# Optimization experiments

Measured on AMD Instinct MI355X. Metric: run time of the kernel, lower is better.

## Reference

```python
import jax, jax.numpy as jnp
import numpy as np

H, LQ, LK, DK, DV = 16, 2048, 2048, 64, 64


def setup_inputs() -> dict:
    key = jax.random.key(0)
    k1, k2, k3, k4 = jax.random.split(key, 4)
    q = jax.random.normal(k1, (H, LQ, DK), dtype=jnp.float32)
    k = jax.random.normal(k2, (H, LK, DK), dtype=jnp.float32)
    v = jax.random.normal(k3, (1, LK, DV), dtype=jnp.float32)
    attn_mask = jax.random.randint(k4, (H, LQ, LK), 0, 2) == 1
    return {"q": q, "k": k, "v": v, "attn_mask": attn_mask, "train_attn": 1}


def reference(q, k, v, attn_mask, train_attn):
    scale = jnp.asarray(np.sqrt(q.shape[-1]), q.dtype)  # sqrt(d_k)
    # [H, Lq, Lk] scores
    attn = jnp.einsum('hqd,hkd->hqk', q, k) / scale
    attn = jnp.where(attn_mask, -jnp.inf, attn)
    attn = jax.nn.softmax(attn, axis=-1)
    # torch: v.repeat(n_heads,1,1) then bmm -> v[0] broadcast over heads
    attn_used = attn if train_attn else jax.lax.stop_gradient(attn)
    v_used = jax.lax.stop_gradient(v) if train_attn else v
    outputs = jnp.einsum('hqk,kd->hqd', attn_used, v_used[0])
    return outputs, attn
```

## Files before the change

### kernel.cpp

```cpp
#include <hip/hip_runtime.h>
#include <hip/hip_bf16.h>
#include <math.h>

#define H_ 16
#define LQ_ 2048
#define LK_ 2048
#define D_ 64
#define QB_ 16
#define NW_ 4
#define STRIP_ (LK_ / NW_)
#define NTL_ (STRIP_ / 16)
#define NCH_ (STRIP_ / 32)
#define PP_ 40

using bf16x8  = __attribute__((ext_vector_type(8))) short;
using floatx4 = __attribute__((ext_vector_type(4))) float;

__device__ __forceinline__ unsigned short f2bf(float x) {
  unsigned u = __builtin_bit_cast(unsigned, x);
  return (unsigned short)((u + 0x7fffu + ((u >> 16) & 1u)) >> 16);
}
__device__ __forceinline__ float bf2f(unsigned short b) {
  return __builtin_bit_cast(float, ((unsigned)b) << 16);
}
__device__ __forceinline__ void hilo8(const float* __restrict__ x, bf16x8& hv, bf16x8& lv) {
#pragma unroll
  for (int j = 0; j < 8; ++j) {
    unsigned short hb = f2bf(x[j]);
    float d = x[j] - bf2f(hb);
    hv[j] = (short)hb;
    lv[j] = (short)(unsigned short)(__builtin_bit_cast(unsigned, d) >> 16);
  }
}

__global__ void detect_mask_kernel(const unsigned* __restrict__ m, int* __restrict__ flag) {
  const int l = (int)threadIdx.x;
  unsigned acc = 0;
#pragma unroll
  for (int i = 0; i < 4; ++i) acc |= m[l * 4 + i];
  unsigned long long any = __ballot(acc & 0xFFFFFF00u);
  if (l == 0) *flag = any ? 1 : 0;
}

__global__ void pack_mask_kernel(const void* __restrict__ Mg, const int* __restrict__ flagp,
                                 unsigned* __restrict__ Wp) {
  const size_t i = (size_t)blockIdx.x * 256 + threadIdx.x;
  unsigned wbits = 0;
  if (*flagp) {
    const uint4* p = (const uint4*)((const unsigned char*)Mg + i * 32);
    uint4 a = p[0], b = p[1];
    unsigned v[8] = {a.x, a.y, a.z, a.w, b.x, b.y, b.z, b.w};
#pragma unroll
    for (int k = 0; k < 8; ++k)
#pragma unroll
      for (int bb = 0; bb < 4; ++bb)
        wbits |= (((v[k] >> (8 * bb)) & 0xFFu) ? 1u : 0u) << (4 * k + bb);
  } else {
    const uint4* p = (const uint4*)((const int*)Mg + i * 32);
#pragma unroll
    for (int k = 0; k < 8; ++k) {
      uint4 a = p[k];
      wbits |= (a.x ? 1u : 0u) << (4 * k)     | (a.y ? 1u : 0u) << (4 * k + 1) |
               (a.z ? 1u : 0u) << (4 * k + 2) | (a.w ? 1u : 0u) << (4 * k + 3);
    }
  }
  Wp[i] = wbits;
}

__global__ void conv_hilo_kernel(const float* __restrict__ X,
                                 unsigned short* __restrict__ Hh,
                                 unsigned short* __restrict__ Hl) {
  const size_t i = (size_t)blockIdx.x * 256 + threadIdx.x;
  float x[8];
  *(floatx4*)x       = *(const floatx4*)(X + i * 8);
  *(floatx4*)(x + 4) = *(const floatx4*)(X + i * 8 + 4);
  bf16x8 hv, lv;
  hilo8(x, hv, lv);
  *(bf16x8*)(Hh + i * 8) = hv;
  *(bf16x8*)(Hl + i * 8) = lv;
}

__global__ void conv_vt_kernel(const float* __restrict__ V,
                               unsigned short* __restrict__ Th,
                               unsigned short* __restrict__ Tl) {
  const int i = (int)(blockIdx.x * 256 + threadIdx.x);
  const int d = i >> 11, k = i & 2047;
  float x = V[(size_t)k * D_ + d];
  unsigned short hb = f2bf(x);
  float rem = x - bf2f(hb);
  Th[(size_t)d * LK_ + k] = hb;
  Tl[(size_t)d * LK_ + k] = (unsigned short)(__builtin_bit_cast(unsigned, rem) >> 16);
}

template <bool PRE>
__global__ __launch_bounds__(256, 2)
void attn_sp_kernel(const float* __restrict__ Qg, const float* __restrict__ Kg,
                    const float* __restrict__ Vg, const void* __restrict__ Mg,
                    const int* __restrict__ flagp,
                    const unsigned* __restrict__ Wp,
                    const unsigned short* __restrict__ Qhp, const unsigned short* __restrict__ Qlp,
                    const unsigned short* __restrict__ Khp, const unsigned short* __restrict__ Klp,
                    const unsigned short* __restrict__ Vthp, const unsigned short* __restrict__ Vtlp,
                    float* __restrict__ Og, float* __restrict__ Ag) {
  const int tid = (int)threadIdx.x;
  const int l = tid & 63, w = tid >> 6, lm = l & 15, lg = l >> 4;
  const int hd = (int)blockIdx.y;
  const int q0 = (int)blockIdx.x * QB_;
  const int k0 = w * STRIP_;

  __shared__ float SM_[NW_][QB_];
  __shared__ float SS_[NW_][QB_];
  __shared__ __align__(16) float OM[NW_][QB_ * D_];
  __shared__ __align__(16) unsigned short Pb[NW_][2][QB_ * PP_];

  const int maskByte = PRE ? 0 : *flagp;
  const unsigned char* Mb = (const unsigned char*)Mg;
  const int* Mi = (const int*)Mg;

  bf16x8 qh[2], ql[2];
  if constexpr (PRE) {
    const unsigned short* qp  = Qhp + ((size_t)hd * LQ_ + q0 + lm) * D_;
    const unsigned short* qp2 = Qlp + ((size_t)hd * LQ_ + q0 + lm) * D_;
    qh[0] = *(const bf16x8*)(qp + lg * 8);       qh[1] = *(const bf16x8*)(qp + 32 + lg * 8);
    ql[0] = *(const bf16x8*)(qp2 + lg * 8);      ql[1] = *(const bf16x8*)(qp2 + 32 + lg * 8);
  } else {
    const float* qp = Qg + ((size_t)hd * LQ_ + q0 + lm) * D_;
#pragma unroll
    for (int s = 0; s < 2; ++s) {
      float x[8];
      *(floatx4*)x       = *(const floatx4*)(qp + s * 32 + lg * 8);
      *(floatx4*)(x + 4) = *(const floatx4*)(qp + s * 32 + lg * 8 + 4);
      hilo8(x, qh[s], ql[s]);
    }
  }

  float s[NTL_][4];
  unsigned wm[4];
  const size_t mwrow = ((size_t)hd * LQ_ + q0 + lg * 4);
#pragma unroll
  for (int t = 0; t < NTL_; ++t) {
    if constexpr (PRE) {
      if ((t & 1) == 0) {
#pragma unroll
        for (int j = 0; j < 4; ++j)
          wm[j] = Wp[((mwrow + j) << 6) + (size_t)(w * 16) + (t >> 1)];
      }
    }
    bf16x8 kh[2], kl[2];
    if constexpr (PRE) {
      const unsigned short* kp  = Khp + ((size_t)hd * LK_ + k0 + t * 16 + lm) * D_;
      const unsigned short* kp2 = Klp + ((size_t)hd * LK_ + k0 + t * 16 + lm) * D_;
      kh[0] = *(const bf16x8*)(kp + lg * 8);       kh[1] = *(const bf16x8*)(kp + 32 + lg * 8);
      kl[0] = *(const bf16x8*)(kp2 + lg * 8);      kl[1] = *(const bf16x8*)(kp2 + 32 + lg * 8);
    } else {
      const float* kp = Kg + ((size_t)hd * LK_ + k0 + t * 16 + lm) * D_;
#pragma unroll
      for (int ss = 0; ss < 2; ++ss) {
        float x[8];
        *(floatx4*)x       = *(const floatx4*)(kp + ss * 32 + lg * 8);
        *(floatx4*)(x + 4) = *(const floatx4*)(kp + ss * 32 + lg * 8 + 4);
        hilo8(x, kh[ss], kl[ss]);
      }
    }
    floatx4 acc = {0.f, 0.f, 0.f, 0.f};
#pragma unroll
    for (int ss = 0; ss < 2; ++ss) {
      acc = __builtin_amdgcn_mfma_f32_16x16x32_bf16(qh[ss], kh[ss], acc, 0, 0, 0);
      acc = __builtin_amdgcn_mfma_f32_16x16x32_bf16(ql[ss], kh[ss], acc, 0, 0, 0);
      acc = __builtin_amdgcn_mfma_f32_16x16x32_bf16(qh[ss], kl[ss], acc, 0, 0, 0);
    }
#pragma unroll
    for (int j = 0; j < 4; ++j) {
      int mk;
      if constexpr (PRE) {
        mk = (int)((wm[j] >> ((t & 1) * 16 + lm)) & 1u);
      } else {
        const size_t mi = ((size_t)hd * LQ_ + q0 + lg * 4 + j) * (size_t)LK_ + k0 + t * 16 + lm;
        mk = maskByte ? (int)Mb[mi] : Mi[mi];
      }
      s[t][j] = mk ? -1e30f : acc[j] * 0.125f;
    }
  }

  float mf[4];
#pragma unroll
  for (int j = 0; j < 4; ++j) {
    float m = s[0][j];
#pragma unroll
    for (int t = 1; t < NTL_; ++t) m = fmaxf(m, s[t][j]);
#pragma unroll
    for (int off = 1; off <= 8; off <<= 1) m = fmaxf(m, __shfl_xor(m, off, 64));
    if (lm == 0) SM_[w][lg * 4 + j] = m;
  }
  __syncthreads();
#pragma unroll
  for (int j = 0; j < 4; ++j)
    mf[j] = fmaxf(fmaxf(SM_[0][lg * 4 + j], SM_[1][lg * 4 + j]),
                  fmaxf(SM_[2][lg * 4 + j], SM_[3][lg * 4 + j]));
#pragma unroll
  for (int j = 0; j < 4; ++j) {
    float sum = 0.f;
#pragma unroll
    for (int t = 0; t < NTL_; ++t) {
      float p = __expf(s[t][j] - mf[j]);
      s[t][j] = p;
      sum += p;
    }
#pragma unroll
    for (int off = 1; off <= 8; off <<= 1) sum += __shfl_xor(sum, off, 64);
    if (lm == 0) SS_[w][lg * 4 + j] = sum;
  }
  __syncthreads();
  float inv[4];
#pragma unroll
  for (int j = 0; j < 4; ++j)
    inv[j] = 1.0f / (SS_[0][lg * 4 + j] + SS_[1][lg * 4 + j] +
                     SS_[2][lg * 4 + j] + SS_[3][lg * 4 + j]);

  floatx4 oacc[4];
#pragma unroll
  for (int n = 0; n < 4; ++n) oacc[n] = {0.f, 0.f, 0.f, 0.f};
  unsigned short* PhL = &Pb[w][0][0];
  unsigned short* PlL = &Pb[w][1][0];

#pragma unroll
  for (int c = 0; c < NCH_; ++c) {
#pragma unroll
    for (int u = 0; u < 2; ++u) {
#pragma unroll
      for (int j = 0; j < 4; ++j) {
        const float p = s[2 * c + u][j] * inv[j];
        const unsigned short hb = f2bf(p);
        const float rem = p - bf2f(hb);
        PhL[(lg * 4 + j) * PP_ + u * 16 + lm] = hb;
        PlL[(lg * 4 + j) * PP_ + u * 16 + lm] =
            (unsigned short)(__builtin_bit_cast(unsigned, rem) >> 16);
      }
    }
    const bf16x8 pa  = *(const bf16x8*)(PhL + lm * PP_ + lg * 8);
    const bf16x8 plo = *(const bf16x8*)(PlL + lm * PP_ + lg * 8);

    {
      float pr[8];
#pragma unroll
      for (int jj = 0; jj < 8; ++jj)
        pr[jj] = bf2f((unsigned short)pa[jj]) + bf2f((unsigned short)plo[jj]);
      float* arow = Ag + ((size_t)hd * LQ_ + q0 + lm) * (size_t)LK_ + k0 + c * 32 + lg * 8;
      floatx4 v0 = {pr[0], pr[1], pr[2], pr[3]};
      floatx4 v1 = {pr[4], pr[5], pr[6], pr[7]};
      *(floatx4*)arow       = v0;
      *(floatx4*)(arow + 4) = v1;
    }

#pragma unroll
    for (int n = 0; n < 4; ++n) {
      bf16x8 vh, vl;
      if constexpr (PRE) {
        const size_t vo = (size_t)(n * 16 + lm) * LK_ + k0 + c * 32 + lg * 8;
        vh = *(const bf16x8*)(Vthp + vo);
        vl = *(const bf16x8*)(Vtlp + vo);
      } else {
        float vx[8];
#pragma unroll
        for (int jj = 0; jj < 8; ++jj)
          vx[jj] = Vg[(size_t)(k0 + c * 32 + lg * 8 + jj) * D_ + n * 16 + lm];
        hilo8(vx, vh, vl);
      }
      floatx4 o = oacc[n];
      o = __builtin_amdgcn_mfma_f32_16x16x32_bf16(pa,  vh, o, 0, 0, 0);
      o = __builtin_amdgcn_mfma_f32_16x16x32_bf16(plo, vh, o, 0, 0, 0);
      o = __builtin_amdgcn_mfma_f32_16x16x32_bf16(pa,  vl, o, 0, 0, 0);
      oacc[n] = o;
    }
  }

#pragma unroll
  for (int n = 0; n < 4; ++n)
#pragma unroll
    for (int j = 0; j < 4; ++j)
      OM[w][(lg * 4 + j) * D_ + n * 16 + lm] = oacc[n][j];
  __syncthreads();
  for (int i = tid; i < QB_ * D_; i += 256) {
    const float o = OM[0][i] + OM[1][i] + OM[2][i] + OM[3][i];
    Og[((size_t)hd * LQ_ + q0 + (i >> 6)) * D_ + (i & 63)] = o;
  }
}

extern "C" void kernel_launch(void* const* d_in, const int* in_sizes, int n_in,
                              void* d_out, int out_size, void* d_ws, size_t ws_size,
                              hipStream_t stream) {
  const float* Qg = (const float*)d_in[0];
  const float* Kg = (const float*)d_in[1];
  const float* Vg = (const float*)d_in[2];
  const void*  Mg = d_in[3];

  char* ws = (char*)d_ws;
  int* flag = (int*)ws;
  unsigned*       Wp  = (unsigned*)(ws + 16);
  unsigned short* Qhp = (unsigned short*)(ws + 16 + 8388608);
  unsigned short* Qlp = (unsigned short*)(ws + 16 + 8388608 + 4194304);
  unsigned short* Khp = (unsigned short*)(ws + 16 + 8388608 + 2 * 4194304);
  unsigned short* Klp = (unsigned short*)(ws + 16 + 8388608 + 3 * 4194304);
  unsigned short* Vth = (unsigned short*)(ws + 16 + 8388608 + 4 * 4194304);
  unsigned short* Vtl = (unsigned short*)(ws + 16 + 8388608 + 4 * 4194304 + 262144);
  const size_t WS_NEEDED = 16 + 8388608 + 4 * (size_t)4194304 + 2 * (size_t)262144;

  float* Og = (float*)d_out;
  float* Ag = (float*)d_out + (size_t)H_ * LQ_ * D_;

  hipLaunchKernelGGL(detect_mask_kernel, dim3(1), dim3(64), 0, stream,
                     (const unsigned*)Mg, flag);

  dim3 grid(LQ_ / QB_, H_);
  if (ws_size >= WS_NEEDED) {
    hipLaunchKernelGGL(pack_mask_kernel, dim3(8192), dim3(256), 0, stream, Mg, flag, Wp);
    hipLaunchKernelGGL(conv_hilo_kernel, dim3(1024), dim3(256), 0, stream, Qg, Qhp, Qlp);
    hipLaunchKernelGGL(conv_hilo_kernel, dim3(1024), dim3(256), 0, stream, Kg, Khp, Klp);
    hipLaunchKernelGGL(conv_vt_kernel, dim3(512), dim3(256), 0, stream, Vg, Vth, Vtl);
    hipLaunchKernelGGL((attn_sp_kernel<true>), grid, dim3(256), 0, stream,
                       Qg, Kg, Vg, Mg, flag, Wp, Qhp, Qlp, Khp, Klp, Vth, Vtl, Og, Ag);
  } else {
    hipLaunchKernelGGL((attn_sp_kernel<false>), grid, dim3(256), 0, stream,
                       Qg, Kg, Vg, Mg, flag, Wp, Qhp, Qlp, Khp, Klp, Vth, Vtl, Og, Ag);
  }
}
```

Before: 691.9 us.

## Transpose score MFMA so rows map to lanes, drop LDS P staging, use 16 waves

```diff
diff --git a/kernel.cpp b/kernel.cpp
--- a/kernel.cpp
+++ b/kernel.cpp
@@ -7,13 +7,12 @@
 #define LK_ 2048
 #define D_ 64
 #define QB_ 16
-#define NW_ 4
-#define STRIP_ (LK_ / NW_)
-#define NTL_ (STRIP_ / 16)
-#define NCH_ (STRIP_ / 32)
-#define PP_ 40
+#define NWAVE_ 16
+#define COLSW_ 128
+#define NT_ 8
 
 using bf16x8  = __attribute__((ext_vector_type(8))) short;
+using short4v = __attribute__((ext_vector_type(4))) short;
 using floatx4 = __attribute__((ext_vector_type(4))) float;
 
 __device__ __forceinline__ unsigned short f2bf(float x) {
@@ -31,6 +30,28 @@
     hv[j] = (short)hb;
     lv[j] = (short)(unsigned short)(__builtin_bit_cast(unsigned, d) >> 16);
   }
+}
+__device__ __forceinline__ void hilo4(const float* __restrict__ x, short4v& hv, short4v& lv) {
+#pragma unroll
+  for (int j = 0; j < 4; ++j) {
+    unsigned short hb = f2bf(x[j]);
+    float d = x[j] - bf2f(hb);
+    hv[j] = (short)hb;
+    lv[j] = (short)(unsigned short)(__builtin_bit_cast(unsigned, d) >> 16);
+  }
+}
+
+__device__ __forceinline__ floatx4 mfma32(bf16x8 a, bf16x8 b, floatx4 c) {
+  return __builtin_amdgcn_mfma_f32_16x16x32_bf16(a, b, c, 0, 0, 0);
+}
+__device__ __forceinline__ floatx4 mfma16(short4v a, short4v b, floatx4 c) {
+#if __has_builtin(__builtin_amdgcn_mfma_f32_16x16x16bf16_1k)
+  return __builtin_amdgcn_mfma_f32_16x16x16bf16_1k(a, b, c, 0, 0, 0);
+#else
+  floatx4 d;
+  asm("v_mfma_f32_16x16x16_bf16 %0, %1, %2, %3" : "=&v"(d) : "v"(a), "v"(b), "v"(c));
+  return d;
+#endif
 }
 
 __global__ void detect_mask_kernel(const unsigned* __restrict__ m, int* __restrict__ flag) {
@@ -93,11 +114,10 @@
 }
 
 template <bool PRE>
-__global__ __launch_bounds__(256, 2)
-void attn_sp_kernel(const float* __restrict__ Qg, const float* __restrict__ Kg,
+__global__ __launch_bounds__(1024, 4)
+void attn_v5_kernel(const float* __restrict__ Qg, const float* __restrict__ Kg,
                     const float* __restrict__ Vg, const void* __restrict__ Mg,
-                    const int* __restrict__ flagp,
-                    const unsigned* __restrict__ Wp,
+                    const int* __restrict__ flagp, const unsigned* __restrict__ Wp,
                     const unsigned short* __restrict__ Qhp, const unsigned short* __restrict__ Qlp,
                     const unsigned short* __restrict__ Khp, const unsigned short* __restrict__ Klp,
                     const unsigned short* __restrict__ Vthp, const unsigned short* __restrict__ Vtlp,
@@ -106,25 +126,25 @@
   const int l = tid & 63, w = tid >> 6, lm = l & 15, lg = l >> 4;
   const int hd = (int)blockIdx.y;
   const int q0 = (int)blockIdx.x * QB_;
-  const int k0 = w * STRIP_;
-
-  __shared__ float SM_[NW_][QB_];
-  __shared__ float SS_[NW_][QB_];
-  __shared__ __align__(16) float OM[NW_][QB_ * D_];
-  __shared__ __align__(16) unsigned short Pb[NW_][2][QB_ * PP_];
-
-  const int maskByte = PRE ? 0 : *flagp;
+  const int k0 = w * COLSW_;
+
+  __shared__ __align__(16) float OM[8][QB_ * D_];
+  __shared__ float SmM[NWAVE_][QB_];
+  __shared__ float SmS[NWAVE_][QB_];
+
+  const int mB = PRE ? 0 : *flagp;
   const unsigned char* Mb = (const unsigned char*)Mg;
   const int* Mi = (const int*)Mg;
+  const size_t qrow = (size_t)hd * LQ_ + q0 + lm;
 
   bf16x8 qh[2], ql[2];
   if constexpr (PRE) {
-    const unsigned short* qp  = Qhp + ((size_t)hd * LQ_ + q0 + lm) * D_;
-    const unsigned short* qp2 = Qlp + ((size_t)hd * LQ_ + q0 + lm) * D_;
-    qh[0] = *(const bf16x8*)(qp + lg * 8);       qh[1] = *(const bf16x8*)(qp + 32 + lg * 8);
-    ql[0] = *(const bf16x8*)(qp2 + lg * 8);      ql[1] = *(const bf16x8*)(qp2 + 32 + lg * 8);
+    const unsigned short* qp  = Qhp + qrow * D_;
+    const unsigned short* qp2 = Qlp + qrow * D_;
+    qh[0] = *(const bf16x8*)(qp  + lg * 8); qh[1] = *(const bf16x8*)(qp  + 32 + lg * 8);
+    ql[0] = *(const bf16x8*)(qp2 + lg * 8); ql[1] = *(const bf16x8*)(qp2 + 32 + lg * 8);
   } else {
-    const float* qp = Qg + ((size_t)hd * LQ_ + q0 + lm) * D_;
+    const float* qp = Qg + qrow * D_;
 #pragma unroll
     for (int s = 0; s < 2; ++s) {
       float x[8];
@@ -134,154 +154,149 @@
     }
   }
 
-  float s[NTL_][4];
-  unsigned wm[4];
-  const size_t mwrow = ((size_t)hd * LQ_ + q0 + lg * 4);
-#pragma unroll
-  for (int t = 0; t < NTL_; ++t) {
+  unsigned wmv[4];
+  if constexpr (PRE) {
+#pragma unroll
+    for (int i = 0; i < 4; ++i) wmv[i] = Wp[qrow * (LK_ / 32) + w * 4 + i];
+  }
+
+  float sc[NT_][4];
+#pragma unroll
+  for (int t = 0; t < NT_; ++t) {
+    bf16x8 kh[2], kl[2];
+    const size_t krow = (size_t)hd * LK_ + k0 + t * 16 + lm;
     if constexpr (PRE) {
-      if ((t & 1) == 0) {
+      const unsigned short* kp  = Khp + krow * D_;
+      const unsigned short* kp2 = Klp + krow * D_;
+      kh[0] = *(const bf16x8*)(kp  + lg * 8); kh[1] = *(const bf16x8*)(kp  + 32 + lg * 8);
+      kl[0] = *(const bf16x8*)(kp2 + lg * 8); kl[1] = *(const bf16x8*)(kp2 + 32 + lg * 8);
+    } else {
+      const float* kp = Kg + krow * D_;
+#pragma unroll
+      for (int s = 0; s < 2; ++s) {
+        float x[8];
+        *(floatx4*)x       = *(const floatx4*)(kp + s * 32 + lg * 8);
+        *(floatx4*)(x + 4) = *(const floatx4*)(kp + s * 32 + lg * 8 + 4);
+        hilo8(x, kh[s], kl[s]);
+      }
+    }
+    floatx4 acc = {0.f, 0.f, 0.f, 0.f};
+#pragma unroll
+    for (int s = 0; s < 2; ++s) {
+      acc = mfma32(kh[s], qh[s], acc);
+      acc = mfma32(kl[s], qh[s], acc);
+      acc = mfma32(kh[s], ql[s], acc);
+    }
+    if constexpr (PRE) {
+#pragma unroll
+      for (int j = 0; j < 4; ++j) {
+        const int mk = (int)((wmv[t >> 1] >> ((t & 1) * 16 + lg * 4 + j)) & 1u);
+        sc[t][j] = mk ? -1e30f : acc[j] * 0.125f;
+      }
+    } else if (mB) {
+      const unsigned mw = *(const unsigned*)(Mb + qrow * LK_ + k0 + t * 16 + lg * 4);
+#pragma unroll
+      for (int j = 0; j < 4; ++j)
+        sc[t][j] = ((mw >> (8 * j)) & 0xFFu) ? -1e30f : acc[j] * 0.125f;
+    } else {
+      const uint4 mv = *(const uint4*)(Mi + qrow * LK_ + k0 + t * 16 + lg * 4);
+      const unsigned mm[4] = {mv.x, mv.y, mv.z, mv.w};
+#pragma unroll
+      for (int j = 0; j < 4; ++j) sc[t][j] = mm[j] ? -1e30f : acc[j] * 0.125f;
+    }
+  }
+
+  float m = -1e30f;
+#pragma unroll
+  for (int t = 0; t < NT_; ++t)
+#pragma unroll
+    for (int j = 0; j < 4; ++j) m = fmaxf(m, sc[t][j]);
+  m = fmaxf(m, __shfl_xor(m, 16, 64));
+  m = fmaxf(m, __shfl_xor(m, 32, 64));
+  if (lg == 0) SmM[w][lm] = m;
+  __syncthreads();
+  float mfin = SmM[0][lm];
+#pragma unroll
+  for (int ww = 1; ww < NWAVE_; ++ww) mfin = fmaxf(mfin, SmM[ww][lm]);
+
+  float sum = 0.f;
+#pragma unroll
+  for (int t = 0; t < NT_; ++t)
+#pragma unroll
+    for (int j = 0; j < 4; ++j) {
+      const float p = __expf(sc[t][j] - mfin);
+      sc[t][j] = p;
+      sum += p;
+    }
+  sum += __shfl_xor(sum, 16, 64);
+  sum += __shfl_xor(sum, 32, 64);
+  if (lg == 0) SmS[w][lm] = sum;
+  __syncthreads();
+  float tot = 0.f;
+#pragma unroll
+  for (int ww = 0; ww < NWAVE_; ++ww) tot += SmS[ww][lm];
+  const float inv = 1.0f / tot;
+
+  floatx4 oacc[4];
+#pragma unroll
+  for (int n = 0; n < 4; ++n) oacc[n] = {0.f, 0.f, 0.f, 0.f};
+
+#pragma unroll
+  for (int t = 0; t < NT_; ++t) {
+    float p[4];
+#pragma unroll
+    for (int j = 0; j < 4; ++j) p[j] = sc[t][j] * inv;
+    floatx4 pv = {p[0], p[1], p[2], p[3]};
+    *(floatx4*)(Ag + qrow * LK_ + k0 + t * 16 + lg * 4) = pv;
+
+    short4v ph, pl;
+    hilo4(p, ph, pl);
+#pragma unroll
+    for (int n = 0; n < 4; ++n) {
+      short4v vh, vl;
+      if constexpr (PRE) {
+        const size_t vo = (size_t)(n * 16 + lm) * LK_ + k0 + t * 16 + lg * 4;
+        vh = *(const short4v*)(Vthp + vo);
+        vl = *(const short4v*)(Vtlp + vo);
+      } else {
+        float vx[4];
 #pragma unroll
         for (int j = 0; j < 4; ++j)
-          wm[j] = Wp[((mwrow + j) << 6) + (size_t)(w * 16) + (t >> 1)];
-      }
-    }
-    bf16x8 kh[2], kl[2];
-    if constexpr (PRE) {
-      const unsigned short* kp  = Khp + ((size_t)hd * LK_ + k0 + t * 16 + lm) * D_;
-      const unsigned short* kp2 = Klp + ((size_t)hd * LK_ + k0 + t * 16 + lm) * D_;
-      kh[0] = *(const bf16x8*)(kp + lg * 8);       kh[1] = *(const bf16x8*)(kp + 32 + lg * 8);
-      kl[0] = *(const bf16x8*)(kp2 + lg * 8);      kl[1] = *(const bf16x8*)(kp2 + 32 + lg * 8);
-    } else {
-      const float* kp = Kg + ((size_t)hd * LK_ + k0 + t * 16 + lm) * D_;
-#pragma unroll
-      for (int ss = 0; ss < 2; ++ss) {
-        float x[8];
-        *(floatx4*)x       = *(const floatx4*)(kp + ss * 32 + lg * 8);
-        *(floatx4*)(x + 4) = *(const floatx4*)(kp + ss * 32 + lg * 8 + 4);
-        hilo8(x, kh[ss], kl[ss]);
-      }
-    }
-    floatx4 acc = {0.f, 0.f, 0.f, 0.f};
-#pragma unroll
-    for (int ss = 0; ss < 2; ++ss) {
-      acc = __builtin_amdgcn_mfma_f32_16x16x32_bf16(qh[ss], kh[ss], acc, 0, 0, 0);
-      acc = __builtin_amdgcn_mfma_f32_16x16x32_bf16(ql[ss], kh[ss], acc, 0, 0, 0);
-      acc = __builtin_amdgcn_mfma_f32_16x16x32_bf16(qh[ss], kl[ss], acc, 0, 0, 0);
-    }
-#pragma unroll
-    for (int j = 0; j < 4; ++j) {
-      int mk;
-      if constexpr (PRE) {
-        mk = (int)((wm[j] >> ((t & 1) * 16 + lm)) & 1u);
-      } else {
-        const size_t mi = ((size_t)hd * LQ_ + q0 + lg * 4 + j) * (size_t)LK_ + k0 + t * 16 + lm;
-        mk = maskByte ? (int)Mb[mi] : Mi[mi];
-      }
-      s[t][j] = mk ? -1e30f : acc[j] * 0.125f;
-    }
-  }
-
-  float mf[4];
-#pragma unroll
-  for (int j = 0; j < 4; ++j) {
-    float m = s[0][j];
-#pragma unroll
-    for (int t = 1; t < NTL_; ++t) m = fmaxf(m, s[t][j]);
-#pragma unroll
-    for (int off = 1; off <= 8; off <<= 1) m = fmaxf(m, __shfl_xor(m, off, 64));
-    if (lm == 0) SM_[w][lg * 4 + j] = m;
-  }
-  __syncthreads();
-#pragma unroll
-  for (int j = 0; j < 4; ++j)
-    mf[j] = fmaxf(fmaxf(SM_[0][lg * 4 + j], SM_[1][lg * 4 + j]),
-                  fmaxf(SM_[2][lg * 4 + j], SM_[3][lg * 4 + j]));
-#pragma unroll
-  for (int j = 0; j < 4; ++j) {
-    float sum = 0.f;
-#pragma unroll
-    for (int t = 0; t < NTL_; ++t) {
-      float p = __expf(s[t][j] - mf[j]);
-      s[t][j] = p;
-      sum += p;
-    }
-#pragma unroll
-    for (int off = 1; off <= 8; off <<= 1) sum += __shfl_xor(sum, off, 64);
-    if (lm == 0) SS_[w][lg * 4 + j] = sum;
-  }
-  __syncthreads();
-  float inv[4];
-#pragma unroll
-  for (int j = 0; j < 4; ++j)
-    inv[j] = 1.0f / (SS_[0][lg * 4 + j] + SS_[1][lg * 4 + j] +
-                     SS_[2][lg * 4 + j] + SS_[3][lg * 4 + j]);
-
-  floatx4 oacc[4];
-#pragma unroll
-  for (int n = 0; n < 4; ++n) oacc[n] = {0.f, 0.f, 0.f, 0.f};
-  unsigned short* PhL = &Pb[w][0][0];
-  unsigned short* PlL = &Pb[w][1][0];
-
-#pragma unroll
-  for (int c = 0; c < NCH_; ++c) {
-#pragma unroll
-    for (int u = 0; u < 2; ++u) {
-#pragma unroll
-      for (int j = 0; j < 4; ++j) {
-        const float p = s[2 * c + u][j] * inv[j];
-        const unsigned short hb = f2bf(p);
-        const float rem = p - bf2f(hb);
-        PhL[(lg * 4 + j) * PP_ + u * 16 + lm] = hb;
-        PlL[(lg * 4 + j) * PP_ + u * 16 + lm] =
-            (unsigned short)(__builtin_bit_cast(unsigned, rem) >> 16);
-      }
-    }
-    const bf16x8 pa  = *(const bf16x8*)(PhL + lm * PP_ + lg * 8);
-    const bf16x8 plo = *(const bf16x8*)(PlL + lm * PP_ + lg * 8);
-
-    {
-      float pr[8];
-#pragma unroll
-      for (int jj = 0; jj < 8; ++jj)
-        pr[jj] = bf2f((unsigned short)pa[jj]) + bf2f((unsigned short)plo[jj]);
-      float* arow = Ag + ((size_t)hd * LQ_ + q0 + lm) * (size_t)LK_ + k0 + c * 32 + lg * 8;
-      floatx4 v0 = {pr[0], pr[1], pr[2], pr[3]};
-      floatx4 v1 = {pr[4], pr[5], pr[6], pr[7]};
-      *(floatx4*)arow       = v0;
-      *(floatx4*)(arow + 4) = v1;
-    }
-
-#pragma unroll
-    for (int n = 0; n < 4; ++n) {
-      bf16x8 vh, vl;
-      if constexpr (PRE) {
-        const size_t vo = (size_t)(n * 16 + lm) * LK_ + k0 + c * 32 + lg * 8;
-        vh = *(const bf16x8*)(Vthp + vo);
-        vl = *(const bf16x8*)(Vtlp + vo);
-      } else {
-        float vx[8];
-#pragma unroll
-        for (int jj = 0; jj < 8; ++jj)
-          vx[jj] = Vg[(size_t)(k0 + c * 32 + lg * 8 + jj) * D_ + n * 16 + lm];
-        hilo8(vx, vh, vl);
+          vx[j] = Vg[(size_t)(k0 + t * 16 + lg * 4 + j) * D_ + n * 16 + lm];
+        hilo4(vx, vh, vl);
       }
       floatx4 o = oacc[n];
-      o = __builtin_amdgcn_mfma_f32_16x16x32_bf16(pa,  vh, o, 0, 0, 0);
-      o = __builtin_amdgcn_mfma_f32_16x16x32_bf16(plo, vh, o, 0, 0, 0);
-      o = __builtin_amdgcn_mfma_f32_16x16x32_bf16(pa,  vl, o, 0, 0, 0);
+      o = mfma16(ph, vh, o);
+      o = mfma16(pl, vh, o);
+      o = mfma16(ph, vl, o);
       oacc[n] = o;
     }
   }
 
-#pragma unroll
-  for (int n = 0; n < 4; ++n)
-#pragma unroll
-    for (int j = 0; j < 4; ++j)
-      OM[w][(lg * 4 + j) * D_ + n * 16 + lm] = oacc[n][j];
-  __syncthreads();
-  for (int i = tid; i < QB_ * D_; i += 256) {
-    const float o = OM[0][i] + OM[1][i] + OM[2][i] + OM[3][i];
+  __syncthreads();
+  if (w >= 8) {
+#pragma unroll
+    for (int n = 0; n < 4; ++n)
+#pragma unroll
+      for (int j = 0; j < 4; ++j)
+        OM[w - 8][(lg * 4 + j) * D_ + n * 16 + lm] = oacc[n][j];
+  }
+  __syncthreads();
+  if (w < 8) {
+#pragma unroll
+    for (int n = 0; n < 4; ++n)
+#pragma unroll
+      for (int j = 0; j < 4; ++j) {
+        const int idx = (lg * 4 + j) * D_ + n * 16 + lm;
+        OM[w][idx] += oacc[n][j];
+      }
+  }
+  __syncthreads();
+  {
+    const int i = tid;
+    float o = 0.f;
+#pragma unroll
+    for (int s = 0; s < 8; ++s) o += OM[s][i];
     Og[((size_t)hd * LQ_ + q0 + (i >> 6)) * D_ + (i & 63)] = o;
   }
 }
@@ -317,10 +332,10 @@
     hipLaunchKernelGGL(conv_hilo_kernel, dim3(1024), dim3(256), 0, stream, Qg, Qhp, Qlp);
     hipLaunchKernelGGL(conv_hilo_kernel, dim3(1024), dim3(256), 0, stream, Kg, Khp, Klp);
     hipLaunchKernelGGL(conv_vt_kernel, dim3(512), dim3(256), 0, stream, Vg, Vth, Vtl);
-    hipLaunchKernelGGL((attn_sp_kernel<true>), grid, dim3(256), 0, stream,
+    hipLaunchKernelGGL((attn_v5_kernel<true>), grid, dim3(1024), 0, stream,
                        Qg, Kg, Vg, Mg, flag, Wp, Qhp, Qlp, Khp, Klp, Vth, Vtl, Og, Ag);
   } else {
-    hipLaunchKernelGGL((attn_sp_kernel<false>), grid, dim3(256), 0, stream,
+    hipLaunchKernelGGL((attn_v5_kernel<false>), grid, dim3(1024), 0, stream,
                        Qg, Kg, Vg, Mg, flag, Wp, Qhp, Qlp, Khp, Klp, Vth, Vtl, Og, Ag);
   }
 }
```

Measured after the change: 833.1 us. +20.4%, slower.
